# Kernel tuning notes

Measured on AMD Instinct MI355X. Metric: run time of the kernel, lower is better.

## Reference

```python
import jax, jax.numpy as jnp
import numpy as np

EPS_NORM = 1e-12   # F.normalize default eps
EPS_ABS = 1e-08


def _l2_normalize(x, axis):
    n = jnp.sqrt(jnp.sum(x * x, axis=axis, keepdims=True))
    return x / jnp.maximum(n, EPS_NORM)


def setup_inputs() -> dict:
    key = jax.random.key(0)
    k1, k2 = jax.random.split(key)
    B, D, H, W = 32, 256, 32, 32
    S = 2048
    features = jax.random.normal(k1, (B, D, H, W), dtype=jnp.float32)
    memory = jax.random.truncated_normal(k2, -2.0, 2.0, (S, D), dtype=jnp.float32) * 0.02
    return {"features": features, "memory": memory}


def reference(features, memory):
    shrink_threshold = 0.0025
    shrink_gamma = 2.0
    temperature = 0.05
    B, D, H, W = features.shape
    S = memory.shape[0]

    # (B,D,H,W) -> (B*H*W, D)
    query = jnp.transpose(features, (0, 2, 3, 1)).reshape(B * H * W, D)

    # addressing: cosine similarity / temperature -> softmax over slots
    q = _l2_normalize(query, axis=1)
    m = _l2_normalize(memory, axis=1)
    sim = (q @ m.T) / temperature                      # [N, S]
    weights = jax.nn.softmax(sim, axis=1)

    # retrieval + soft shrinkage
    retrieved = weights @ memory                       # [N, D]
    a = jnp.abs(retrieved)
    lam = jnp.clip(shrink_gamma * shrink_threshold / (a + EPS_ABS), 0.0, 1.0)
    retrieved = jnp.sign(retrieved) * jax.nn.relu(a * (1.0 - lam))

    # entropy of addressing weights
    entropy = -jnp.mean(jnp.sum(weights * jnp.log(weights + EPS_ABS), axis=1))

    retrieved = jnp.transpose(retrieved.reshape(B, H, W, D), (0, 3, 1, 2))
    weights_image = weights.reshape(B, H * W, S).mean(axis=1)
    return retrieved, entropy, weights_image
```

## Files before the change

### kernel.cpp

```cpp
#include <hip/hip_runtime.h>
#include <cstdint>
#include <cstddef>

#define D_DIM 256
#define S_SLOTS 2048
#define HW_PIX 1024
#define OUT_ENT_IDX 8388608
#define OUT_WIMG_IDX 8388609

#define BUFA_OFF(b) ((b) * 32768)
#define BUFB_OFF(b) (65536 + (b) * 32768)
#define WIMG_OFF    131072
#define FUSED_DYN   139264

#define LOG2E_20 28.853900817779268f
#define LN2F     0.6931471805599453f

using short8 = __attribute__((ext_vector_type(8))) short;
using f32x4  = __attribute__((ext_vector_type(4))) float;

__device__ __forceinline__ unsigned short f2bf(float x) {
    union { float f; unsigned u; } v; v.f = x;
    unsigned r = v.u + 0x7FFF + ((v.u >> 16) & 1);
    return (unsigned short)(r >> 16);
}
__device__ __forceinline__ unsigned pack2(float lo, float hi) {
    return (unsigned)f2bf(lo) | ((unsigned)f2bf(hi) << 16);
}
__device__ __forceinline__ void gload16(const void* g, void* l) {
    __builtin_amdgcn_global_load_lds(
        (const __attribute__((address_space(1))) unsigned int*)g,
        (__attribute__((address_space(3))) unsigned int*)l, 16, 0, 0);
}

__global__ __launch_bounds__(64) void k_prep(const float* __restrict__ mem,
                                             unsigned short* __restrict__ mhatg,
                                             unsigned short* __restrict__ mblkg) {
    __shared__ float lm[8 * 257];
    __shared__ float scl[8];
    const int l = threadIdx.x, blk = blockIdx.x;
    const int tile = blk >> 3, oct = blk & 7;
    const int s0 = tile * 64 + oct * 8;
    const float* src = mem + (size_t)s0 * D_DIM;
#pragma unroll
    for (int i = 0; i < 8; ++i) {
        const int f4 = i * 64 + l;
        const int r = f4 >> 6, dq = (f4 & 63) * 4;
        const float4 v = reinterpret_cast<const float4*>(src)[f4];
        float* p = lm + r * 257 + dq;
        p[0] = v.x; p[1] = v.y; p[2] = v.z; p[3] = v.w;
    }
    __syncthreads();
    {
        const int r = l >> 3, pp = l & 7;
        float ss = 0.f;
#pragma unroll 8
        for (int d = 0; d < 32; ++d) { const float v = lm[r * 257 + pp * 32 + d]; ss += v * v; }
        ss += __shfl_xor(ss, 1); ss += __shfl_xor(ss, 2); ss += __shfl_xor(ss, 4);
        if (pp == 0) scl[r] = LOG2E_20 / fmaxf(sqrtf(ss), 1e-12f);
    }
    __syncthreads();
#pragma unroll
    for (int i = 0; i < 4; ++i) {
        const int c = i * 64 + l, r = c >> 5, k = c & 31;
        const int s_g = s0 + r;
        const float sc = scl[r];
        const float* p = lm + r * 257 + ((k ^ (s_g & 7)) * 8);
        union { short8 s; unsigned short h[8]; } o;
#pragma unroll
        for (int j = 0; j < 8; ++j) o.h[j] = f2bf(p[j] * sc);
        *reinterpret_cast<short8*>((char*)mhatg + (size_t)s_g * 512 + k * 16) = o.s;
    }
#pragma unroll
    for (int i = 0; i < 4; ++i) {
        const int d = i * 64 + l;
        const int k = oct ^ (d & 7);
        union { short8 s; unsigned short h[8]; } o;
#pragma unroll
        for (int j = 0; j < 8; ++j) o.h[j] = f2bf(lm[j * 257 + d]);
        *reinterpret_cast<short8*>((char*)mblkg + (size_t)tile * 32768 + d * 128 + k * 16) = o.s;
    }
}

__device__ __forceinline__ void qkt(const char* mh, const short8 (&qfrag)[2][8],
                                    int srow, int g, int l15, f32x4 (&acc)[2][2]) {
#pragma unroll
    for (int kk = 0; kk < 8; ++kk) {
        const int c0 = ((4 * kk + g) ^ (l15 & 7)) << 4;
        const short8 a0 = *reinterpret_cast<const short8*>(mh + srow * 512 + c0);
        const short8 a1 = *reinterpret_cast<const short8*>(mh + (srow + 16) * 512 + c0);
        acc[0][0] = __builtin_amdgcn_mfma_f32_16x16x32_bf16(a0, qfrag[0][kk], acc[0][0], 0, 0, 0);
        acc[0][1] = __builtin_amdgcn_mfma_f32_16x16x32_bf16(a0, qfrag[1][kk], acc[0][1], 0, 0, 0);
        acc[1][0] = __builtin_amdgcn_mfma_f32_16x16x32_bf16(a1, qfrag[0][kk], acc[1][0], 0, 0, 0);
        acc[1][1] = __builtin_amdgcn_mfma_f32_16x16x32_bf16(a1, qfrag[1][kk], acc[1][1], 0, 0, 0);
    }
}

__global__ __launch_bounds__(512, 2) void k_fused(
    const float* __restrict__ feat, const char* __restrict__ mhat_g,
    const char* __restrict__ mblk_g, float* __restrict__ out)
{
    extern __shared__ char dyn[];
    __shared__ float sm_norm[512];
    __shared__ float qs_lds[128];
    __shared__ float zb[2][4][2][16];
    __shared__ float ub[2][4][2][16];
    __shared__ float rZbuf[128];
    __shared__ float entb[4];

    const int tid  = threadIdx.x;
    const int lane = tid & 63;
    const int w    = tid >> 6;
    const int wq   = w & 3;
    const int ws   = w >> 2;
    const int l15  = lane & 15;
    const int g    = (lane >> 4) & 3;
    const int blk  = blockIdx.x;
    const int b    = blk >> 3;
    const int p0   = (blk & 7) * 128;
    const float* fbase = feat + (size_t)b * (D_DIM * HW_PIX);
    float* wimg_l = reinterpret_cast<float*>(dyn + WIMG_OFF);

    auto stageA = [&](int st, int buf) {
        const char* gsrc = mhat_g + (size_t)st * 32768;
        char* ldst = dyn + BUFA_OFF(buf);
#pragma unroll
        for (int i = 0; i < 4; ++i)
            gload16(gsrc + tid * 16 + i * 8192, ldst + tid * 16 + i * 8192);
    };
    auto stageB = [&](int st, int buf) {
        const char* gsrc = mblk_g + (size_t)st * 32768;
        char* ldst = dyn + BUFB_OFF(buf);
#pragma unroll
        for (int i = 0; i < 4; ++i)
            gload16(gsrc + tid * 16 + i * 8192, ldst + tid * 16 + i * 8192);
    };
    auto stageA2 = [&](int st, int buf) {
        const char* gsrc = mhat_g + (size_t)st * 32768;
        char* ldst = dyn + BUFB_OFF(buf);
#pragma unroll
        for (int i = 0; i < 4; ++i)
            gload16(gsrc + tid * 16 + i * 8192, ldst + tid * 16 + i * 8192);
    };

    stageA(0, 0); stageB(0, 0);

#pragma unroll
    for (int i = 0; i < 4; ++i) wimg_l[i * 512 + tid] = 0.f;

    {
        const int dp = tid >> 7, pp = tid & 127;
        const float* fp = fbase + (size_t)(dp * 64) * HW_PIX + p0 + pp;
        float ss = 0.f;
#pragma unroll 8
        for (int d = 0; d < 64; ++d) { const float v = fp[(size_t)d * HW_PIX]; ss += v * v; }
        sm_norm[dp * 128 + pp] = ss;
    }
    __syncthreads();
    if (tid < 128) {
        const float n2 = sm_norm[tid] + sm_norm[128 + tid] + sm_norm[256 + tid] + sm_norm[384 + tid];
        qs_lds[tid] = 1.0f / fmaxf(sqrtf(n2), 1e-12f);
    }
    __syncthreads();

    short8 qfrag[2][8];
#pragma unroll
    for (int tq = 0; tq < 2; ++tq) {
        const int q = 32 * wq + 16 * tq + l15;
        const float qs = qs_lds[q];
        const float* fq = fbase + p0 + q;
#pragma unroll
        for (int kk = 0; kk < 8; ++kk) {
            union { short8 s; unsigned u[4]; } fr;
#pragma unroll
            for (int jp = 0; jp < 4; ++jp) {
                const int d = 32 * kk + 8 * g + 2 * jp;
                fr.u[jp] = pack2(fq[(size_t)d * HW_PIX] * qs, fq[(size_t)(d + 1) * HW_PIX] * qs);
            }
            qfrag[tq][kk] = fr.s;
        }
    }

    const int srow = 32 * ws + l15;

    float Zp[2] = {0.f, 0.f}, Up[2] = {0.f, 0.f};
    f32x4 acc_o[2][16] = {};
    __syncthreads();
    int cur = 0;
    for (int st = 0; st < 32; ++st) {
        if (st < 31) { stageA(st + 1, cur ^ 1); stageB(st + 1, cur ^ 1); }
        f32x4 acc[2][2] = {};
        qkt(dyn + BUFA_OFF(cur), qfrag, srow, g, l15, acc);
        float ev[2][2][4];
#pragma unroll
        for (int ts = 0; ts < 2; ++ts)
#pragma unroll
            for (int tq = 0; tq < 2; ++tq)
#pragma unroll
                for (int r = 0; r < 4; ++r) {
                    const float sim2 = acc[ts][tq][r];
                    const float e = exp2f(sim2);
                    ev[ts][tq][r] = e;
                    Zp[tq] += e; Up[tq] += e * sim2;
                }
        short8 pfrag[2];
#pragma unroll
        for (int tq = 0; tq < 2; ++tq) {
            const unsigned u00 = pack2(ev[0][tq][0], ev[0][tq][1]);
            const unsigned u01 = pack2(ev[0][tq][2], ev[0][tq][3]);
            const unsigned u10 = pack2(ev[1][tq][0], ev[1][tq][1]);
            const unsigned u11 = pack2(ev[1][tq][2], ev[1][tq][3]);
            const int sA = l15 + 32 * (g & 1);
            const int sB = sA + 16;
            const unsigned a00 = __shfl((int)u00, sA), a10 = __shfl((int)u10, sA);
            const unsigned a01 = __shfl((int)u01, sA), a11 = __shfl((int)u11, sA);
            const unsigned b00 = __shfl((int)u00, sB), b10 = __shfl((int)u10, sB);
            const unsigned b01 = __shfl((int)u01, sB), b11 = __shfl((int)u11, sB);
            const bool hi = (lane & 32) != 0;
            union { short8 s; unsigned u[4]; } fr;
            fr.u[0] = hi ? a10 : a00;
            fr.u[1] = hi ? a11 : a01;
            fr.u[2] = hi ? b10 : b00;
            fr.u[3] = hi ? b11 : b01;
            pfrag[tq] = fr.s;
        }
        const char* mb = dyn + BUFB_OFF(cur);
        const int cswz = (((4 * ws + g) ^ (l15 & 7)) << 4);
#pragma unroll
        for (int Dt = 0; Dt < 16; ++Dt) {
            const int d = 16 * Dt + l15;
            const short8 bf = *reinterpret_cast<const short8*>(mb + d * 128 + cswz);
            acc_o[0][Dt] = __builtin_amdgcn_mfma_f32_16x16x32_bf16(pfrag[0], bf, acc_o[0][Dt], 0, 0, 0);
            acc_o[1][Dt] = __builtin_amdgcn_mfma_f32_16x16x32_bf16(pfrag[1], bf, acc_o[1][Dt], 0, 0, 0);
        }
        __syncthreads();
        cur ^= 1;
    }

#pragma unroll
    for (int tq = 0; tq < 2; ++tq) {
        Zp[tq] += __shfl_xor(Zp[tq], 16); Zp[tq] += __shfl_xor(Zp[tq], 32);
        Up[tq] += __shfl_xor(Up[tq], 16); Up[tq] += __shfl_xor(Up[tq], 32);
    }
    if (lane < 16) {
#pragma unroll
        for (int tq = 0; tq < 2; ++tq) {
            zb[ws][wq][tq][lane] = Zp[tq];
            ub[ws][wq][tq][lane] = Up[tq];
        }
    }
    __syncthreads();
    {
        float Zf[2], Uf[2], rZ[2];
#pragma unroll
        for (int tq = 0; tq < 2; ++tq) {
            Zf[tq] = Zp[tq] + zb[1 - ws][wq][tq][l15];
            Uf[tq] = Up[tq] + ub[1 - ws][wq][tq][l15];
            rZ[tq] = 1.0f / Zf[tq];
        }
        if (ws == 0 && lane < 16) {
            rZbuf[32 * wq + l15]      = rZ[0];
            rZbuf[32 * wq + 16 + l15] = rZ[1];
            float ent = 0.f;
#pragma unroll
            for (int tq = 0; tq < 2; ++tq) ent += __logf(Zf[tq]) - LN2F * Uf[tq] * rZ[tq];
            ent += __shfl_xor(ent, 1); ent += __shfl_xor(ent, 2);
            ent += __shfl_xor(ent, 4); ent += __shfl_xor(ent, 8);
            if (lane == 0) entb[wq] = ent;
        }
    }
    __syncthreads();
    if (tid == 0)
        atomicAdd(out + OUT_ENT_IDX, (entb[0] + entb[1] + entb[2] + entb[3]) * (1.0f / 32768.0f));

    stageA2(0, 0);

    float rZq[2][4];
#pragma unroll
    for (int tq = 0; tq < 2; ++tq)
#pragma unroll
        for (int r = 0; r < 4; ++r)
            rZq[tq][r] = rZbuf[32 * wq + 16 * tq + 4 * g + r];

#pragma unroll
    for (int Dt = 0; Dt < 16; ++Dt) {
        if (ws == 1) {
#pragma unroll
            for (int tq = 0; tq < 2; ++tq)
                *reinterpret_cast<f32x4*>(dyn + ((wq * 2 + tq) * 64 + lane) * 16) = acc_o[tq][Dt];
        }
        __syncthreads();
        if (ws == 0) {
#pragma unroll
            for (int tq = 0; tq < 2; ++tq) {
                const f32x4 other = *reinterpret_cast<const f32x4*>(dyn + ((wq * 2 + tq) * 64 + lane) * 16);
#pragma unroll
                for (int r = 0; r < 4; ++r) {
                    const float o = (acc_o[tq][Dt][r] + other[r]) * rZq[tq][r];
                    const float a = fabsf(o);
                    const float lam = fminf(0.005f / (a + 1e-8f), 1.0f);
                    const float val = copysignf(a * (1.0f - lam), o);
                    const int q = 32 * wq + 16 * tq + 4 * g + r;
                    *reinterpret_cast<float*>(dyn + 8192 + q * 84 + l15 * 4) = val;
                }
            }
        }
        __syncthreads();
#pragma unroll
        for (int i = 0; i < 4; ++i) {
            const int flat = i * 512 + tid;
            const int dd = flat >> 7, q = flat & 127;
            const float val = *reinterpret_cast<const float*>(dyn + 8192 + q * 84 + dd * 4);
            out[((size_t)b * 256 + Dt * 16 + dd) * HW_PIX + p0 + q] = val;
        }
        __syncthreads();
    }

    {
        float rzq[2][4];
#pragma unroll
        for (int tq = 0; tq < 2; ++tq)
#pragma unroll
            for (int r = 0; r < 4; ++r)
                rzq[tq][r] = rZbuf[32 * wq + 16 * tq + 4 * g + r] * (1.0f / 1024.0f);

        int cur2 = 0;
        for (int st = 0; st < 32; ++st) {
            if (st < 31) stageA2(st + 1, cur2 ^ 1);
            const char* mh = dyn + BUFB_OFF(cur2);
            f32x4 a2[2][2] = {};
#pragma unroll
            for (int kk = 0; kk < 8; ++kk) {
                const int c0 = ((4 * kk + g) ^ (l15 & 7)) << 4;
                const short8 m0 = *reinterpret_cast<const short8*>(mh + srow * 512 + c0);
                const short8 m1 = *reinterpret_cast<const short8*>(mh + (srow + 16) * 512 + c0);
                a2[0][0] = __builtin_amdgcn_mfma_f32_16x16x32_bf16(qfrag[0][kk], m0, a2[0][0], 0, 0, 0);
                a2[0][1] = __builtin_amdgcn_mfma_f32_16x16x32_bf16(qfrag[1][kk], m0, a2[0][1], 0, 0, 0);
                a2[1][0] = __builtin_amdgcn_mfma_f32_16x16x32_bf16(qfrag[0][kk], m1, a2[1][0], 0, 0, 0);
                a2[1][1] = __builtin_amdgcn_mfma_f32_16x16x32_bf16(qfrag[1][kk], m1, a2[1][1], 0, 0, 0);
            }
#pragma unroll
            for (int sb = 0; sb < 2; ++sb) {
                float v = 0.f;
#pragma unroll
                for (int tq = 0; tq < 2; ++tq)
#pragma unroll
                    for (int r = 0; r < 4; ++r)
                        v += exp2f(a2[sb][tq][r]) * rzq[tq][r];
                v += __shfl_xor(v, 16);
                v += __shfl_xor(v, 32);
                if (lane < 16)
                    atomicAdd(&wimg_l[st * 64 + 32 * ws + 16 * sb + l15], v);
            }
            __syncthreads();
            cur2 ^= 1;
        }
    }
    {
        float* wimg_gb = out + OUT_WIMG_IDX + (size_t)b * S_SLOTS;
#pragma unroll
        for (int i = 0; i < 4; ++i) {
            const int s = i * 512 + tid;
            atomicAdd(wimg_gb + s, wimg_l[s]);
        }
    }
}

extern "C" void kernel_launch(void* const* d_in, const int* in_sizes, int n_in,
                              void* d_out, int out_size, void* d_ws, size_t ws_size,
                              hipStream_t stream) {
    const float* feat = (const float*)d_in[0];
    const float* mem  = (const float*)d_in[1];
    float* out = (float*)d_out;

    unsigned short* mhat_g = (unsigned short*)d_ws;
    unsigned short* mblk_g = (unsigned short*)((char*)d_ws + (1 << 20));

    hipMemsetAsync((char*)d_out + (size_t)OUT_ENT_IDX * 4, 0,
                   (size_t)(1 + 32 * S_SLOTS) * 4, stream);

    k_prep<<<256, 64, 0, stream>>>(mem, mhat_g, mblk_g);

    hipFuncSetAttribute((const void*)k_fused,
                        hipFuncAttributeMaxDynamicSharedMemorySize, FUSED_DYN);
    k_fused<<<256, 512, FUSED_DYN, stream>>>(feat, (const char*)mhat_g,
                                             (const char*)mblk_g, out);
}
```

Before: 274.2 us.

## Store softmax probabilities to workspace instead of recomputing QK^T for weights_image

During the main pass the bf16 exp fragments are written to a 128 MB global scratch buffer. The weights_image pass then reads them back and scales by 1/Z, instead of restaging memory tiles and redoing the QK^T MFMAs and exp. This removes the second matmul pass but adds about 128 MB of global writes and reads, and uses bf16-rounded probabilities. It falls back to the old recompute path when the workspace is too small.

Result: faster. 220.9 us (-19.4%).

```diff
diff --git a/kernel.cpp b/kernel.cpp
--- a/kernel.cpp
+++ b/kernel.cpp
@@ -13,6 +13,9 @@
 #define WIMG_OFF    131072
 #define FUSED_DYN   139264
 
+#define PST_BYTES   134217728ULL
+#define WS_NEEDED   ((2ULL << 20) + PST_BYTES)
+
 #define LOG2E_20 28.853900817779268f
 #define LN2F     0.6931471805599453f
 
@@ -23,6 +26,9 @@
     union { float f; unsigned u; } v; v.f = x;
     unsigned r = v.u + 0x7FFF + ((v.u >> 16) & 1);
     return (unsigned short)(r >> 16);
+}
+__device__ __forceinline__ float bf2f(unsigned short h) {
+    union { unsigned u; float f; } v; v.u = ((unsigned)h) << 16; return v.f;
 }
 __device__ __forceinline__ unsigned pack2(float lo, float hi) {
     return (unsigned)f2bf(lo) | ((unsigned)f2bf(hi) << 16);
@@ -96,9 +102,11 @@
     }
 }
 
+template <bool PST>
 __global__ __launch_bounds__(512, 2) void k_fused(
     const float* __restrict__ feat, const char* __restrict__ mhat_g,
-    const char* __restrict__ mblk_g, float* __restrict__ out)
+    const char* __restrict__ mblk_g, char* __restrict__ pst,
+    float* __restrict__ out)
 {
     extern __shared__ char dyn[];
     __shared__ float sm_norm[512];
@@ -224,6 +232,12 @@
             fr.u[3] = hi ? b11 : b01;
             pfrag[tq] = fr.s;
         }
+        if (PST) {
+            char* pdst = pst + (size_t)blk * 524288 + (size_t)st * 16384
+                         + w * 2048 + lane * 16;
+            *reinterpret_cast<short8*>(pdst)        = pfrag[0];
+            *reinterpret_cast<short8*>(pdst + 1024) = pfrag[1];
+        }
         const char* mb = dyn + BUFB_OFF(cur);
         const int cswz = (((4 * ws + g) ^ (l15 & 7)) << 4);
 #pragma unroll
@@ -273,7 +287,7 @@
     if (tid == 0)
         atomicAdd(out + OUT_ENT_IDX, (entb[0] + entb[1] + entb[2] + entb[3]) * (1.0f / 32768.0f));
 
-    stageA2(0, 0);
+    if (!PST) stageA2(0, 0);
 
     float rZq[2][4];
 #pragma unroll
@@ -316,7 +330,32 @@
         __syncthreads();
     }
 
-    {
+    if (PST) {
+        float rz2[2];
+        rz2[0] = rZbuf[32 * wq + l15]      * (1.0f / 1024.0f);
+        rz2[1] = rZbuf[32 * wq + 16 + l15] * (1.0f / 1024.0f);
+        const int grp = lane >> 4;
+        const char* pbase = pst + (size_t)blk * 524288 + w * 2048 + lane * 16;
+        for (int st = 0; st < 32; ++st) {
+            const char* p = pbase + (size_t)st * 16384;
+            union { short8 s; unsigned short h[8]; } e0, e1;
+            e0.s = *reinterpret_cast<const short8*>(p);
+            e1.s = *reinterpret_cast<const short8*>(p + 1024);
+            float v[8];
+#pragma unroll
+            for (int j = 0; j < 8; ++j)
+                v[j] = bf2f(e0.h[j]) * rz2[0] + bf2f(e1.h[j]) * rz2[1];
+#pragma unroll
+            for (int o = 1; o <= 8; o <<= 1)
+#pragma unroll
+                for (int j = 0; j < 8; ++j) v[j] += __shfl_xor(v[j], o);
+            if (l15 == 0) {
+#pragma unroll
+                for (int j = 0; j < 8; ++j)
+                    atomicAdd(&wimg_l[st * 64 + 32 * ws + 8 * grp + j], v[j]);
+            }
+        }
+    } else {
         float rzq[2][4];
 #pragma unroll
         for (int tq = 0; tq < 2; ++tq)
@@ -356,6 +395,8 @@
             cur2 ^= 1;
         }
     }
+
+    __syncthreads();
     {
         float* wimg_gb = out + OUT_WIMG_IDX + (size_t)b * S_SLOTS;
 #pragma unroll
@@ -375,14 +416,22 @@
 
     unsigned short* mhat_g = (unsigned short*)d_ws;
     unsigned short* mblk_g = (unsigned short*)((char*)d_ws + (1 << 20));
+    char*           pst    = (char*)d_ws + (2 << 20);
 
     hipMemsetAsync((char*)d_out + (size_t)OUT_ENT_IDX * 4, 0,
                    (size_t)(1 + 32 * S_SLOTS) * 4, stream);
 
     k_prep<<<256, 64, 0, stream>>>(mem, mhat_g, mblk_g);
 
-    hipFuncSetAttribute((const void*)k_fused,
-                        hipFuncAttributeMaxDynamicSharedMemorySize, FUSED_DYN);
-    k_fused<<<256, 512, FUSED_DYN, stream>>>(feat, (const char*)mhat_g,
-                                             (const char*)mblk_g, out);
-}
+    if (ws_size >= WS_NEEDED) {
+        hipFuncSetAttribute((const void*)k_fused<true>,
+                            hipFuncAttributeMaxDynamicSharedMemorySize, FUSED_DYN);
+        k_fused<true><<<256, 512, FUSED_DYN, stream>>>(
+            feat, (const char*)mhat_g, (const char*)mblk_g, pst, out);
+    } else {
+        hipFuncSetAttribute((const void*)k_fused<false>,
+                            hipFuncAttributeMaxDynamicSharedMemorySize, FUSED_DYN);
+        k_fused<false><<<256, 512, FUSED_DYN, stream>>>(
+            feat, (const char*)mhat_g, (const char*)mblk_g, pst, out);
+    }
+}
```
